# Kernel optimization log

Hardware: AMD Instinct MI355X
Metric: run time of the kernel (lower is better)

## Reference

```python
import jax, jax.numpy as jnp
import numpy as np

CUTOFF = 5.0
NUM_RADIAL = 6
HIDDEN = 128
N_NODES = 100000
N_EDGES = 800000
MAX_Z = 95
P = 6  # envelope_exponent(5) + 1, per PyG Envelope


def _envelope(x):
    # PyG DimeNet Envelope: (1/x + a*x^(p-1) + b*x^p + c*x^(p+1)) * (x < 1)
    a = -(P + 1) * (P + 2) / 2.0   # -28
    b = P * (P + 2)                # 48
    c = -P * (P + 1) / 2.0         # -21
    xp0 = x ** (P - 1)
    xp1 = xp0 * x
    xp2 = xp1 * x
    return (1.0 / x + a * xp0 + b * xp1 + c * xp2) * (x < 1.0)


def setup_inputs():
    key = jax.random.key(0)
    ks = jax.random.split(key, 8)
    z = jax.random.randint(ks[0], (N_NODES,), 0, MAX_Z, dtype=jnp.int32)
    pos = jax.random.normal(ks[1], (N_NODES, 3), dtype=jnp.float32)
    ei = jax.random.randint(ks[2], (2, N_EDGES), 0, N_NODES, dtype=jnp.int32)
    i, j = ei[0], ei[1]
    j = jnp.where(j == i, (j + 1) % N_NODES, j)  # radius_graph emits no self-loops (avoids d=0)
    edge_index = jnp.stack([i, j])
    # BesselBasisLayer learnable frequencies: pi * n
    freq = np.pi * jnp.arange(1, NUM_RADIAL + 1, dtype=jnp.float32)
    s3 = float(np.sqrt(3.0))
    emb_table = jax.random.uniform(ks[3], (MAX_Z, HIDDEN), jnp.float32, -s3, s3)
    W_rbf = jax.random.normal(ks[4], (NUM_RADIAL, HIDDEN), jnp.float32) * (1.0 / np.sqrt(NUM_RADIAL))
    b_rbf = jnp.zeros((HIDDEN,), jnp.float32)
    W_lin = jax.random.normal(ks[5], (3 * HIDDEN, HIDDEN), jnp.float32) * (1.0 / np.sqrt(3 * HIDDEN))
    b_lin = jnp.zeros((HIDDEN,), jnp.float32)
    return {"z": z, "pos": pos, "edge_index": edge_index, "freq": freq,
            "emb_table": emb_table, "W_rbf": W_rbf, "b_rbf": b_rbf,
            "W_lin": W_lin, "b_lin": b_lin}


def reference(z, pos, edge_index, freq, emb_table, W_rbf, b_rbf, W_lin, b_lin):
    n = z.shape[0]
    i, j = edge_index[0], edge_index[1]
    # per-edge distance  [E]
    d = jnp.sqrt(jnp.sum((pos[i] - pos[j]) ** 2, axis=-1))
    # Bessel RBF  [E, num_radial]
    x = d[:, None] / CUTOFF
    rbf = _envelope(x) * jnp.sin(freq * x)
    # DimeNet EmbeddingBlock (act = SiLU/swish)
    h_rbf = jax.nn.silu(rbf @ W_rbf + b_rbf)            # [E, H]
    xz = emb_table[z]                                    # [N, H]
    e_emb = jax.nn.silu(
        jnp.concatenate([xz[i], xz[j], h_rbf], axis=-1) @ W_lin + b_lin
    )                                                    # [E, H]
    # scatter_mean over target node j -> [N, H]
    sums = jax.ops.segment_sum(e_emb, j, num_segments=n)
    cnt = jax.ops.segment_sum(jnp.ones_like(d), j, num_segments=n)
    v_emb = sums / jnp.maximum(cnt, 1.0)[:, None]
    return v_emb  # pool=None -> node-level embeddings
```

## Files before the change

### kernel.cpp

```cpp
#include <hip/hip_runtime.h>
#include <hip/hip_bf16.h>
#include <math.h>

#define HID 128
#define NRAD 6
#define TABN 4096
#define CUTOFF_INV 0.2f
#define MZ 95
#define MZP (MZ + 1)
#define SENTI (MZ << 13)
#define PAD 32
#define OVF_CAP 65536
#define FTR 8
#define LOG2E 1.4426950408889634f
#define LN2   0.6931471805599453f

typedef unsigned int uint32;
typedef __attribute__((ext_vector_type(2))) float f2;

__global__ void zpack_k(const float* __restrict__ pos, const int* __restrict__ z,
                        float4* __restrict__ pos4, int* __restrict__ cnt,
                        int* __restrict__ ovfcnt, int N) {
    int n = blockIdx.x * 256 + threadIdx.x;
    if (blockIdx.x == 0 && threadIdx.x == 0) *ovfcnt = 0;
    if (n < N) {
        float4 p;
        p.x = pos[3 * n];
        p.y = pos[3 * n + 1];
        p.z = pos[3 * n + 2];
        p.w = __int_as_float(z[n]);
        pos4[n] = p;
        cnt[n]  = 0;
    }
}

__global__ void build1(const float* __restrict__ emb, const float* __restrict__ W_lin,
                       const float* __restrict__ freq, const float* __restrict__ W_rbf,
                       const float* __restrict__ b_rbf, const float* __restrict__ b_lin,
                       const int* __restrict__ ei, const float4* __restrict__ pos4,
                       __hip_bfloat16* __restrict__ Tb, float* __restrict__ ftab,
                       int* __restrict__ cnt, int* __restrict__ payload,
                       int* __restrict__ ovfcnt, int2* __restrict__ ovfbuf,
                       int MAXZ, int E) {
    __shared__ float sh[FTR * HID];
    int h   = threadIdx.x;
    int bid = blockIdx.x;
    int nT  = 2 * (MAXZ + 1);
    int nF  = (TABN + FTR) / FTR;
    if (bid < nT) {
        int zz = bid >> 1, s = bid & 1;
        if (zz == MAXZ) {
            Tb[(size_t)(s * (MAXZ + 1) + zz) * HID + h] = __float2bfloat16(-86.5f);
            return;
        }
        sh[h] = emb[zz * HID + h];
        __syncthreads();
        const float* W = W_lin + (size_t)s * HID * HID;
        float acc = (s == 0) ? b_lin[h] : 0.f;
#pragma unroll 8
        for (int k = 0; k < HID; ++k) acc = fmaf(sh[k], W[k * HID + h], acc);
        Tb[(size_t)(s * (MAXZ + 1) + zz) * HID + h] = __float2bfloat16(acc * LOG2E);
    } else if (bid < nT + nF) {
        int t0 = (bid - nT) * FTR;
        for (int r = 0; r < FTR; ++r) {
            int t = t0 + r;
            float rbf[NRAD];
            if (t == 0) {
#pragma unroll
                for (int k = 0; k < NRAD; ++k) rbf[k] = freq[k];
            } else if (t >= TABN) {
#pragma unroll
                for (int k = 0; k < NRAD; ++k) rbf[k] = 0.f;
            } else {
                float x  = (float)t / (float)TABN;
                float x2 = x * x, x5 = x2 * x2 * x;
                float env = 1.f / x + x5 * (-28.f + x * (48.f + x * (-21.f)));
#pragma unroll
                for (int k = 0; k < NRAD; ++k) rbf[k] = env * sinf(freq[k] * x);
            }
            float pre = b_rbf[h];
#pragma unroll
            for (int k = 0; k < NRAD; ++k) pre = fmaf(rbf[k], W_rbf[k * HID + h], pre);
            sh[r * HID + h] = pre / (1.f + __expf(-pre));
        }
        __syncthreads();
        const float* W3 = W_lin + (size_t)2 * HID * HID;
        float acc[FTR];
#pragma unroll
        for (int r = 0; r < FTR; ++r) acc[r] = 0.f;
#pragma unroll 4
        for (int k = 0; k < HID; ++k) {
            float w = W3[k * HID + h];
#pragma unroll
            for (int r = 0; r < FTR; ++r) acc[r] = fmaf(sh[r * HID + k], w, acc[r]);
        }
        for (int r = 0; r < FTR; ++r) {
            int t = t0 + r;
            if (t <= TABN) ftab[(size_t)t * HID + h] = acc[r] * LOG2E;
        }
    } else {
        int t  = (bid - nT - nF) * HID + h;
        int Eh = (E + 1) >> 1;
        if (t < Eh) {
            int  e1   = t + Eh;
            bool has1 = e1 < E;
            int i0 = ei[t],  j0 = ei[E + t];
            int i1 = has1 ? ei[e1] : i0, j1 = has1 ? ei[E + e1] : j0;
            float4 a0 = pos4[i0], b0 = pos4[j0];
            float4 a1 = pos4[i1], b1 = pos4[j1];

            float dx0 = a0.x - b0.x, dy0 = a0.y - b0.y, dz0 = a0.z - b0.z;
            float d0  = sqrtf(dx0 * dx0 + dy0 * dy0 + dz0 * dz0);
            float u0  = fminf(d0 * CUTOFF_INV, 1.0f) * (float)TABN;
            int   ti0 = (int)(u0 + 0.5f);
            if (ti0 > TABN) ti0 = TABN;
            int pl0 = ti0 | (__float_as_int(a0.w) << 13);
            int r0  = atomicAdd(&cnt[j0], 1);
            if (r0 < PAD) payload[(size_t)j0 * PAD + r0] = pl0;
            else { int o = atomicAdd(ovfcnt, 1); if (o < OVF_CAP) ovfbuf[o] = make_int2(j0, pl0); }

            if (has1) {
                float dx1 = a1.x - b1.x, dy1 = a1.y - b1.y, dz1 = a1.z - b1.z;
                float d1  = sqrtf(dx1 * dx1 + dy1 * dy1 + dz1 * dz1);
                float u1  = fminf(d1 * CUTOFF_INV, 1.0f) * (float)TABN;
                int   ti1 = (int)(u1 + 0.5f);
                if (ti1 > TABN) ti1 = TABN;
                int pl1 = ti1 | (__float_as_int(a1.w) << 13);
                int r1  = atomicAdd(&cnt[j1], 1);
                if (r1 < PAD) payload[(size_t)j1 * PAD + r1] = pl1;
                else { int o = atomicAdd(ovfcnt, 1); if (o < OVF_CAP) ovfbuf[o] = make_int2(j1, pl1); }
            }
        }
    }
}

__device__ __forceinline__ float exp2neg(float x) {
    float r; asm("v_exp_f32 %0, -%1" : "=v"(r) : "v"(x)); return r;
}

#define RL(pv_, idx_) __builtin_amdgcn_readlane((pv_), (idx_))

#define FLOAD(pl_) (*(const f2*)((const char*)ftab + (uint32)((((pl_) & 0x1FFF) << 9) + fbyte)))

#define TLA(pl_) sT[((((pl_) >> 13) & 0x7F) << 6) + lane]

#define COMPUTE(f_, ua_) do {                                                  \
    f2 A_, P_, E_, R_;                                                         \
    A_.x = __uint_as_float((ua_) << 16);                                       \
    A_.y = __uint_as_float((ua_) & 0xFFFF0000u);                               \
    P_ = (A_ + Bv) + f_;                                  \
    E_.x = exp2neg(P_.x);  E_.y = exp2neg(P_.y);                               \
    E_ = E_ + onev;                                              \
    R_.x = __builtin_amdgcn_rcpf(E_.x);                                        \
    R_.y = __builtin_amdgcn_rcpf(E_.y);                                        \
    acc = __builtin_elementwise_fma(P_, R_, acc);            \
} while (0)

__launch_bounds__(1024)
__global__ void gather_k(const int* __restrict__ cnt, const int* __restrict__ payload,
                         const uint32* __restrict__ Tb32, const float* __restrict__ ftab,
                         const int* __restrict__ z,
                         const int* __restrict__ ovfcnt, const int2* __restrict__ ovfbuf,
                         float* __restrict__ out, int N) {
    __shared__ uint32 sT[MZP * (HID / 2)];
    int tid = threadIdx.x;
    for (int k = tid; k < MZP * (HID / 2); k += 1024) sT[k] = Tb32[k];
    __syncthreads();

    const uint32* T2g = Tb32 + MZP * (HID / 2);
    int lane = tid & 63;
    int l32  = lane & 31;
    int wv   = __builtin_amdgcn_readfirstlane(tid >> 6);
    uint32 fbyte = (uint32)lane << 3;
    f2 onev; onev.x = 1.f; onev.y = 1.f;
    int nov  = __builtin_amdgcn_readfirstlane(*ovfcnt);
    if (nov > OVF_CAP) nov = OVF_CAP;
    int nW = gridDim.x << 4;

    int n = (blockIdx.x << 4) + wv;
    int degC = 0, plvC = SENTI; uint32 ubC = 0;
    if (n < N) {
        degC = __builtin_amdgcn_readfirstlane(cnt[n]);
        plvC = payload[(size_t)n * PAD + l32];
        int zn = __builtin_amdgcn_readfirstlane(z[n]);
        ubC  = T2g[(zn << 6) + lane];
    }

    while (n < N) {
        int n2 = n + nW;
        int degN = 0, plvN = SENTI; uint32 ubN = 0;
        if (n2 < N) {
            degN = __builtin_amdgcn_readfirstlane(cnt[n2]);
            plvN = payload[(size_t)n2 * PAD + l32];
            int zn2 = __builtin_amdgcn_readfirstlane(z[n2]);
            ubN  = T2g[(zn2 << 6) + lane];
        }

        int deg = degC;
        int cb  = deg < PAD ? deg : PAD;
        int plv = (l32 < cb) ? plvC : SENTI;
        f2 Bv;
        Bv.x = __uint_as_float(ubC << 16);
        Bv.y = __uint_as_float(ubC & 0xFFFF0000u);

        f2 acc; acc.x = 0.f; acc.y = 0.f;
        if (cb > 0) {
            int pl0 = RL(plv, 0), pl1 = RL(plv, 1), pl2 = RL(plv, 2);
            f2 g0 = FLOAD(pl0), g1 = FLOAD(pl1), g2 = FLOAD(pl2);
            uint32 ua0 = TLA(pl0);
            uint32 ua1 = TLA(pl1);
#pragma unroll 4
            for (int k = 0; k < cb; ++k) {
                int pl3 = RL(plv, k + 3);
                f2 g3 = FLOAD(pl3);
                uint32 ua2 = TLA(pl2);
                COMPUTE(g0, ua0);
                g0 = g1; g1 = g2; g2 = g3;
                ua0 = ua1; ua1 = ua2;
                pl2 = pl3;
            }
        }
        if (deg > PAD && nov > 0) {
            for (int o = 0; o < nov; ++o) {
                int2 v = ovfbuf[o];
                int jn = __builtin_amdgcn_readfirstlane(v.x);
                if (jn == n) {
                    int pl = __builtin_amdgcn_readfirstlane(v.y);
                    f2 f_ = FLOAD(pl);
                    uint32 ua_ = TLA(pl);
                    COMPUTE(f_, ua_);
                }
            }
        }
        float s = (deg > 0) ? LN2 / (float)deg : 0.0f;
        f2 o2; o2.x = acc.x * s; o2.y = acc.y * s;
        *(f2*)(out + (size_t)n * HID + (lane << 1)) = o2;
        n = n2; degC = degN; plvC = plvN; ubC = ubN;
    }
}

extern "C" void kernel_launch(void* const* d_in, const int* in_sizes, int n_in,
                              void* d_out, int out_size, void* d_ws, size_t ws_size,
                              hipStream_t stream) {
    const int*   z     = (const int*)d_in[0];
    const float* pos   = (const float*)d_in[1];
    const int*   ei    = (const int*)d_in[2];
    const float* freq  = (const float*)d_in[3];
    const float* emb   = (const float*)d_in[4];
    const float* W_rbf = (const float*)d_in[5];
    const float* b_rbf = (const float*)d_in[6];
    const float* W_lin = (const float*)d_in[7];
    const float* b_lin = (const float*)d_in[8];

    int N    = in_sizes[0];
    int E    = in_sizes[2] / 2;
    int MAXZ = in_sizes[4] / HID;
    float* out = (float*)d_out;

    int N_pad = ((N + 1024) / 1024) * 1024;

    char* ws = (char*)d_ws;
    size_t off = 0;
    auto alloc = [&](size_t bytes) { char* p = ws + off; off = (off + bytes + 255) & ~(size_t)255; return p; };
    int*   cnt     = (int*)alloc((size_t)N_pad * 4);
    int*   ovfcnt  = (int*)alloc(256);
    __hip_bfloat16* Tb = (__hip_bfloat16*)alloc((size_t)2 * (MAXZ + 1) * HID * 2);
    float* ftab    = (float*)alloc((size_t)(TABN + 1) * HID * 4);
    int*   payload = (int*)alloc((size_t)N_pad * PAD * 4);
    int2*  ovfbuf  = (int2*)alloc((size_t)OVF_CAP * 8);
    float4* pos4   = (float4*)alloc((size_t)N_pad * 16);

    zpack_k<<<(N + 255) / 256, 256, 0, stream>>>(pos, z, pos4, cnt, ovfcnt, N);

    int Eh = (E + 1) / 2;
    int nBuild = 2 * (MAXZ + 1) + (TABN + FTR) / FTR + (Eh + HID - 1) / HID;
    build1<<<nBuild, HID, 0, stream>>>(emb, W_lin, freq, W_rbf, b_rbf, b_lin,
                                       ei, pos4, Tb, ftab, cnt, payload,
                                       ovfcnt, ovfbuf, MAXZ, E);
    gather_k<<<512, 1024, 0, stream>>>(cnt, payload, (const uint32*)Tb, ftab, z,
                                       ovfcnt, ovfbuf, out, N);
}
```

Baseline: 180.3 us.

## Pack atom type into count word and deepen gather prefetch pipeline

The node's atom type is stored in the top byte of the per-node counter, so the gather kernel no longer makes a separate dependent load of z per node. The gather loop now prefetches two nodes ahead: counts and payload two iterations out, and the bias row plus first ftab row one iteration out. This is meant to hide global-load latency at node boundaries. It adds register pressure and relies on degrees staying below 2^24.

After: 175.4 us (median of 2 runs). 1.03x faster.

```diff
diff --git a/kernel.cpp b/kernel.cpp
--- a/kernel.cpp
+++ b/kernel.cpp
@@ -24,13 +24,14 @@
     int n = blockIdx.x * 256 + threadIdx.x;
     if (blockIdx.x == 0 && threadIdx.x == 0) *ovfcnt = 0;
     if (n < N) {
+        int zn = z[n];
         float4 p;
         p.x = pos[3 * n];
         p.y = pos[3 * n + 1];
         p.z = pos[3 * n + 2];
-        p.w = __int_as_float(z[n]);
+        p.w = __int_as_float(zn);
         pos4[n] = p;
-        cnt[n]  = 0;
+        cnt[n]  = zn << 24;
     }
 }
 
@@ -115,7 +116,7 @@
             int   ti0 = (int)(u0 + 0.5f);
             if (ti0 > TABN) ti0 = TABN;
             int pl0 = ti0 | (__float_as_int(a0.w) << 13);
-            int r0  = atomicAdd(&cnt[j0], 1);
+            int r0  = atomicAdd(&cnt[j0], 1) & 0xFFFFFF;
             if (r0 < PAD) payload[(size_t)j0 * PAD + r0] = pl0;
             else { int o = atomicAdd(ovfcnt, 1); if (o < OVF_CAP) ovfbuf[o] = make_int2(j0, pl0); }
 
@@ -126,7 +127,7 @@
                 int   ti1 = (int)(u1 + 0.5f);
                 if (ti1 > TABN) ti1 = TABN;
                 int pl1 = ti1 | (__float_as_int(a1.w) << 13);
-                int r1  = atomicAdd(&cnt[j1], 1);
+                int r1  = atomicAdd(&cnt[j1], 1) & 0xFFFFFF;
                 if (r1 < PAD) payload[(size_t)j1 * PAD + r1] = pl1;
                 else { int o = atomicAdd(ovfcnt, 1); if (o < OVF_CAP) ovfbuf[o] = make_int2(j1, pl1); }
             }
@@ -159,7 +160,6 @@
 __launch_bounds__(1024)
 __global__ void gather_k(const int* __restrict__ cnt, const int* __restrict__ payload,
                          const uint32* __restrict__ Tb32, const float* __restrict__ ftab,
-                         const int* __restrict__ z,
                          const int* __restrict__ ovfcnt, const int2* __restrict__ ovfbuf,
                          float* __restrict__ out, int N) {
     __shared__ uint32 sT[MZP * (HID / 2)];
@@ -177,50 +177,64 @@
     if (nov > OVF_CAP) nov = OVF_CAP;
     int nW = gridDim.x << 4;
 
-    int n = (blockIdx.x << 4) + wv;
-    int degC = 0, plvC = SENTI; uint32 ubC = 0;
+    int n  = (blockIdx.x << 4) + wv;
+    int n1 = n + nW;
+
+    int cv0 = 0, plv0 = SENTI; uint32 ub0 = 0;
     if (n < N) {
-        degC = __builtin_amdgcn_readfirstlane(cnt[n]);
-        plvC = payload[(size_t)n * PAD + l32];
-        int zn = __builtin_amdgcn_readfirstlane(z[n]);
-        ubC  = T2g[(zn << 6) + lane];
+        cv0  = __builtin_amdgcn_readfirstlane(cnt[n]);
+        plv0 = payload[(size_t)n * PAD + l32];
+    }
+    int deg0 = cv0 & 0xFFFFFF;
+    int zn0  = ((uint32)cv0) >> 24;
+    int cb0  = deg0 < PAD ? deg0 : PAD;
+    plv0 = (l32 < cb0) ? plv0 : SENTI;
+    if (n < N) ub0 = T2g[(zn0 << 6) + lane];
+    f2 g00 = FLOAD(RL(plv0, 0));
+
+    int cv1 = 0, plv1 = SENTI;
+    if (n1 < N) {
+        cv1  = __builtin_amdgcn_readfirstlane(cnt[n1]);
+        plv1 = payload[(size_t)n1 * PAD + l32];
     }
 
     while (n < N) {
-        int n2 = n + nW;
-        int degN = 0, plvN = SENTI; uint32 ubN = 0;
+        int n2 = n1 + nW;
+        int cv2 = 0, plv2 = SENTI;
         if (n2 < N) {
-            degN = __builtin_amdgcn_readfirstlane(cnt[n2]);
-            plvN = payload[(size_t)n2 * PAD + l32];
-            int zn2 = __builtin_amdgcn_readfirstlane(z[n2]);
-            ubN  = T2g[(zn2 << 6) + lane];
-        }
-
-        int deg = degC;
-        int cb  = deg < PAD ? deg : PAD;
-        int plv = (l32 < cb) ? plvC : SENTI;
+            cv2  = __builtin_amdgcn_readfirstlane(cnt[n2]);
+            plv2 = payload[(size_t)n2 * PAD + l32];
+        }
+        int deg1 = cv1 & 0xFFFFFF;
+        int zn1  = ((uint32)cv1) >> 24;
+        int cb1  = deg1 < PAD ? deg1 : PAD;
+        plv1 = (l32 < cb1) ? plv1 : SENTI;
+        uint32 ub1 = 0;
+        if (n1 < N) ub1 = T2g[(zn1 << 6) + lane];
+        f2 g01 = FLOAD(RL(plv1, 0));
+
         f2 Bv;
-        Bv.x = __uint_as_float(ubC << 16);
-        Bv.y = __uint_as_float(ubC & 0xFFFF0000u);
-
+        Bv.x = __uint_as_float(ub0 << 16);
+        Bv.y = __uint_as_float(ub0 & 0xFFFF0000u);
         f2 acc; acc.x = 0.f; acc.y = 0.f;
-        if (cb > 0) {
-            int pl0 = RL(plv, 0), pl1 = RL(plv, 1), pl2 = RL(plv, 2);
-            f2 g0 = FLOAD(pl0), g1 = FLOAD(pl1), g2 = FLOAD(pl2);
-            uint32 ua0 = TLA(pl0);
-            uint32 ua1 = TLA(pl1);
+        if (cb0 > 0) {
+            f2 g0 = g00;
+            int pl1e = RL(plv0, 1), pl2e = RL(plv0, 2);
+            f2 g1 = FLOAD(pl1e), g2 = FLOAD(pl2e);
+            uint32 ua0 = TLA(RL(plv0, 0));
+            uint32 ua1 = TLA(pl1e);
 #pragma unroll 4
-            for (int k = 0; k < cb; ++k) {
-                int pl3 = RL(plv, k + 3);
+            for (int k = 0; k < cb0; ++k) {
+                int pl3 = RL(plv0, k + 3);
                 f2 g3 = FLOAD(pl3);
-                uint32 ua2 = TLA(pl2);
+                uint32 ua2 = TLA(pl2e);
                 COMPUTE(g0, ua0);
                 g0 = g1; g1 = g2; g2 = g3;
                 ua0 = ua1; ua1 = ua2;
-                pl2 = pl3;
-            }
-        }
-        if (deg > PAD && nov > 0) {
+                pl2e = pl3;
+            }
+        }
+        if (deg0 > PAD && nov > 0) {
             for (int o = 0; o < nov; ++o) {
                 int2 v = ovfbuf[o];
                 int jn = __builtin_amdgcn_readfirstlane(v.x);
@@ -232,10 +246,13 @@
                 }
             }
         }
-        float s = (deg > 0) ? LN2 / (float)deg : 0.0f;
+        float s = (deg0 > 0) ? LN2 / (float)deg0 : 0.0f;
         f2 o2; o2.x = acc.x * s; o2.y = acc.y * s;
         *(f2*)(out + (size_t)n * HID + (lane << 1)) = o2;
-        n = n2; degC = degN; plvC = plvN; ubC = ubN;
+
+        n = n1; n1 = n2;
+        deg0 = deg1; cb0 = cb1; plv0 = plv1; ub0 = ub1; g00 = g01;
+        cv1 = cv2; plv1 = plv2;
     }
 }
 
@@ -277,6 +294,6 @@
     build1<<<nBuild, HID, 0, stream>>>(emb, W_lin, freq, W_rbf, b_rbf, b_lin,
                                        ei, pos4, Tb, ftab, cnt, payload,
                                        ovfcnt, ovfbuf, MAXZ, E);
-    gather_k<<<512, 1024, 0, stream>>>(cnt, payload, (const uint32*)Tb, ftab, z,
+    gather_k<<<512, 1024, 0, stream>>>(cnt, payload, (const uint32*)Tb, ftab,
                                        ovfcnt, ovfbuf, out, N);
 }
```

## Process two nodes per wave in gather, pack z into count, four edges per build thread

Applied to the files above, without the earlier changes.

The gather kernel now interleaves two destination nodes per wavefront, with deeper software prefetch of counts and payloads two iterations ahead, so the exp/rcp chains of the two nodes can overlap memory latency. The atomic-counter word now carries the node's atomic number in its top byte, which removes the separate z load in gather. The edge build phase handles four edges per thread and issues all atomics before the payload stores. Costs are higher register pressure (launch bounds set to 8 waves), load imbalance when the two nodes have different degrees, and a degree field that is now limited to 24 bits.

Result: slower. 185.2 us (+2.7%).

```diff
diff --git a/kernel.cpp b/kernel.cpp
--- a/kernel.cpp
+++ b/kernel.cpp
@@ -24,14 +24,24 @@
     int n = blockIdx.x * 256 + threadIdx.x;
     if (blockIdx.x == 0 && threadIdx.x == 0) *ovfcnt = 0;
     if (n < N) {
+        int zn = z[n];
         float4 p;
         p.x = pos[3 * n];
         p.y = pos[3 * n + 1];
         p.z = pos[3 * n + 2];
-        p.w = __int_as_float(z[n]);
+        p.w = __int_as_float(zn);
         pos4[n] = p;
-        cnt[n]  = 0;
+        cnt[n]  = zn << 24;
     }
+}
+
+__device__ __forceinline__ int mk_pl(float4 a, float4 b) {
+    float dx = a.x - b.x, dy = a.y - b.y, dz = a.z - b.z;
+    float d  = sqrtf(dx * dx + dy * dy + dz * dz);
+    float u  = fminf(d * CUTOFF_INV, 1.0f) * (float)TABN;
+    int   ti = (int)(u + 0.5f);
+    if (ti > TABN) ti = TABN;
+    return ti | (__float_as_int(a.w) << 13);
 }
 
 __global__ void build1(const float* __restrict__ emb, const float* __restrict__ W_lin,
@@ -100,36 +110,38 @@
         }
     } else {
         int t  = (bid - nT - nF) * HID + h;
-        int Eh = (E + 1) >> 1;
-        if (t < Eh) {
-            int  e1   = t + Eh;
-            bool has1 = e1 < E;
+        int Eq = (E + 3) >> 2;
+        if (t < Eq) {
+            int e1 = t + Eq, e2 = t + 2 * Eq, e3 = t + 3 * Eq;
+            bool h1 = e1 < E, h2 = e2 < E, h3 = e3 < E;
             int i0 = ei[t],  j0 = ei[E + t];
-            int i1 = has1 ? ei[e1] : i0, j1 = has1 ? ei[E + e1] : j0;
+            int i1 = h1 ? ei[e1] : i0, j1 = h1 ? ei[E + e1] : j0;
+            int i2 = h2 ? ei[e2] : i0, j2 = h2 ? ei[E + e2] : j0;
+            int i3 = h3 ? ei[e3] : i0, j3 = h3 ? ei[E + e3] : j0;
             float4 a0 = pos4[i0], b0 = pos4[j0];
             float4 a1 = pos4[i1], b1 = pos4[j1];
-
-            float dx0 = a0.x - b0.x, dy0 = a0.y - b0.y, dz0 = a0.z - b0.z;
-            float d0  = sqrtf(dx0 * dx0 + dy0 * dy0 + dz0 * dz0);
-            float u0  = fminf(d0 * CUTOFF_INV, 1.0f) * (float)TABN;
-            int   ti0 = (int)(u0 + 0.5f);
-            if (ti0 > TABN) ti0 = TABN;
-            int pl0 = ti0 | (__float_as_int(a0.w) << 13);
-            int r0  = atomicAdd(&cnt[j0], 1);
+            float4 a2 = pos4[i2], b2 = pos4[j2];
+            float4 a3 = pos4[i3], b3 = pos4[j3];
+            int pl0 = mk_pl(a0, b0), pl1 = mk_pl(a1, b1);
+            int pl2 = mk_pl(a2, b2), pl3 = mk_pl(a3, b3);
+            int r0 =      atomicAdd(&cnt[j0], 1) & 0xFFFFFF;
+            int r1 = h1 ? atomicAdd(&cnt[j1], 1) & 0xFFFFFF : 0;
+            int r2 = h2 ? atomicAdd(&cnt[j2], 1) & 0xFFFFFF : 0;
+            int r3 = h3 ? atomicAdd(&cnt[j3], 1) & 0xFFFFFF : 0;
             if (r0 < PAD) payload[(size_t)j0 * PAD + r0] = pl0;
             else { int o = atomicAdd(ovfcnt, 1); if (o < OVF_CAP) ovfbuf[o] = make_int2(j0, pl0); }
-
-            if (has1) {
-                float dx1 = a1.x - b1.x, dy1 = a1.y - b1.y, dz1 = a1.z - b1.z;
-                float d1  = sqrtf(dx1 * dx1 + dy1 * dy1 + dz1 * dz1);
-                float u1  = fminf(d1 * CUTOFF_INV, 1.0f) * (float)TABN;
-                int   ti1 = (int)(u1 + 0.5f);
-                if (ti1 > TABN) ti1 = TABN;
-                int pl1 = ti1 | (__float_as_int(a1.w) << 13);
-                int r1  = atomicAdd(&cnt[j1], 1);
+            if (h1) {
                 if (r1 < PAD) payload[(size_t)j1 * PAD + r1] = pl1;
                 else { int o = atomicAdd(ovfcnt, 1); if (o < OVF_CAP) ovfbuf[o] = make_int2(j1, pl1); }
             }
+            if (h2) {
+                if (r2 < PAD) payload[(size_t)j2 * PAD + r2] = pl2;
+                else { int o = atomicAdd(ovfcnt, 1); if (o < OVF_CAP) ovfbuf[o] = make_int2(j2, pl2); }
+            }
+            if (h3) {
+                if (r3 < PAD) payload[(size_t)j3 * PAD + r3] = pl3;
+                else { int o = atomicAdd(ovfcnt, 1); if (o < OVF_CAP) ovfbuf[o] = make_int2(j3, pl3); }
+            }
         }
     }
 }
@@ -144,22 +156,21 @@
 
 #define TLA(pl_) sT[((((pl_) >> 13) & 0x7F) << 6) + lane]
 
-#define COMPUTE(f_, ua_) do {                                                  \
+#define COMPUTE(f_, ua_, Bv_, acc_) do {                                       \
     f2 A_, P_, E_, R_;                                                         \
     A_.x = __uint_as_float((ua_) << 16);                                       \
     A_.y = __uint_as_float((ua_) & 0xFFFF0000u);                               \
-    P_ = (A_ + Bv) + f_;                                  \
+    P_ = (A_ + Bv_) + f_;                                 \
     E_.x = exp2neg(P_.x);  E_.y = exp2neg(P_.y);                               \
     E_ = E_ + onev;                                              \
     R_.x = __builtin_amdgcn_rcpf(E_.x);                                        \
     R_.y = __builtin_amdgcn_rcpf(E_.y);                                        \
-    acc = __builtin_elementwise_fma(P_, R_, acc);            \
+    acc_ = __builtin_elementwise_fma(P_, R_, acc_);          \
 } while (0)
 
-__launch_bounds__(1024)
+__launch_bounds__(1024, 8)
 __global__ void gather_k(const int* __restrict__ cnt, const int* __restrict__ payload,
                          const uint32* __restrict__ Tb32, const float* __restrict__ ftab,
-                         const int* __restrict__ z,
                          const int* __restrict__ ovfcnt, const int2* __restrict__ ovfbuf,
                          float* __restrict__ out, int N) {
     __shared__ uint32 sT[MZP * (HID / 2)];
@@ -175,67 +186,100 @@
     f2 onev; onev.x = 1.f; onev.y = 1.f;
     int nov  = __builtin_amdgcn_readfirstlane(*ovfcnt);
     if (nov > OVF_CAP) nov = OVF_CAP;
-    int nW = gridDim.x << 4;
-
-    int n = (blockIdx.x << 4) + wv;
-    int degC = 0, plvC = SENTI; uint32 ubC = 0;
-    if (n < N) {
-        degC = __builtin_amdgcn_readfirstlane(cnt[n]);
-        plvC = payload[(size_t)n * PAD + l32];
-        int zn = __builtin_amdgcn_readfirstlane(z[n]);
-        ubC  = T2g[(zn << 6) + lane];
-    }
-
-    while (n < N) {
-        int n2 = n + nW;
-        int degN = 0, plvN = SENTI; uint32 ubN = 0;
-        if (n2 < N) {
-            degN = __builtin_amdgcn_readfirstlane(cnt[n2]);
-            plvN = payload[(size_t)n2 * PAD + l32];
-            int zn2 = __builtin_amdgcn_readfirstlane(z[n2]);
-            ubN  = T2g[(zn2 << 6) + lane];
-        }
-
-        int deg = degC;
-        int cb  = deg < PAD ? deg : PAD;
-        int plv = (l32 < cb) ? plvC : SENTI;
-        f2 Bv;
-        Bv.x = __uint_as_float(ubC << 16);
-        Bv.y = __uint_as_float(ubC & 0xFFFF0000u);
-
-        f2 acc; acc.x = 0.f; acc.y = 0.f;
-        if (cb > 0) {
-            int pl0 = RL(plv, 0), pl1 = RL(plv, 1), pl2 = RL(plv, 2);
-            f2 g0 = FLOAD(pl0), g1 = FLOAD(pl1), g2 = FLOAD(pl2);
-            uint32 ua0 = TLA(pl0);
-            uint32 ua1 = TLA(pl1);
-#pragma unroll 4
-            for (int k = 0; k < cb; ++k) {
-                int pl3 = RL(plv, k + 3);
-                f2 g3 = FLOAD(pl3);
-                uint32 ua2 = TLA(pl2);
-                COMPUTE(g0, ua0);
-                g0 = g1; g1 = g2; g2 = g3;
-                ua0 = ua1; ua1 = ua2;
-                pl2 = pl3;
-            }
-        }
-        if (deg > PAD && nov > 0) {
+    int nW  = gridDim.x << 4;
+    int nW2 = nW << 1;
+
+    int nA = (blockIdx.x << 4) + wv;
+    int nB = nA + nW;
+
+    int cvA = 0, cvB = 0, plvA = SENTI, plvB = SENTI;
+    if (nA < N) { cvA = __builtin_amdgcn_readfirstlane(cnt[nA]); plvA = payload[(size_t)nA * PAD + l32]; }
+    if (nB < N) { cvB = __builtin_amdgcn_readfirstlane(cnt[nB]); plvB = payload[(size_t)nB * PAD + l32]; }
+    int degA = cvA & 0xFFFFFF, degB = cvB & 0xFFFFFF;
+    int cbA = degA < PAD ? degA : PAD, cbB = degB < PAD ? degB : PAD;
+    plvA = (l32 < cbA) ? plvA : SENTI;
+    plvB = (l32 < cbB) ? plvB : SENTI;
+    uint32 ubA = 0, ubB = 0;
+    if (nA < N) ubA = T2g[((((uint32)cvA) >> 24) << 6) + lane];
+    if (nB < N) ubB = T2g[((((uint32)cvB) >> 24) << 6) + lane];
+    f2 gA00 = FLOAD(RL(plvA, 0));
+    f2 gB00 = FLOAD(RL(plvB, 0));
+
+    int nA1 = nA + nW2, nB1 = nB + nW2;
+    int cvA1 = 0, cvB1 = 0, plvA1 = SENTI, plvB1 = SENTI;
+    if (nA1 < N) { cvA1 = __builtin_amdgcn_readfirstlane(cnt[nA1]); plvA1 = payload[(size_t)nA1 * PAD + l32]; }
+    if (nB1 < N) { cvB1 = __builtin_amdgcn_readfirstlane(cnt[nB1]); plvB1 = payload[(size_t)nB1 * PAD + l32]; }
+
+    while (nA < N) {
+        int nA2 = nA1 + nW2, nB2 = nB1 + nW2;
+        int cvA2 = 0, cvB2 = 0, plvA2 = SENTI, plvB2 = SENTI;
+        if (nA2 < N) { cvA2 = __builtin_amdgcn_readfirstlane(cnt[nA2]); plvA2 = payload[(size_t)nA2 * PAD + l32]; }
+        if (nB2 < N) { cvB2 = __builtin_amdgcn_readfirstlane(cnt[nB2]); plvB2 = payload[(size_t)nB2 * PAD + l32]; }
+        int degA1 = cvA1 & 0xFFFFFF, degB1 = cvB1 & 0xFFFFFF;
+        int cbA1 = degA1 < PAD ? degA1 : PAD, cbB1 = degB1 < PAD ? degB1 : PAD;
+        plvA1 = (l32 < cbA1) ? plvA1 : SENTI;
+        plvB1 = (l32 < cbB1) ? plvB1 : SENTI;
+        uint32 ubA1 = 0, ubB1 = 0;
+        if (nA1 < N) ubA1 = T2g[((((uint32)cvA1) >> 24) << 6) + lane];
+        if (nB1 < N) ubB1 = T2g[((((uint32)cvB1) >> 24) << 6) + lane];
+        f2 gA01 = FLOAD(RL(plvA1, 0));
+        f2 gB01 = FLOAD(RL(plvB1, 0));
+
+        f2 BvA, BvB;
+        BvA.x = __uint_as_float(ubA << 16); BvA.y = __uint_as_float(ubA & 0xFFFF0000u);
+        BvB.x = __uint_as_float(ubB << 16); BvB.y = __uint_as_float(ubB & 0xFFFF0000u);
+        f2 accA; accA.x = 0.f; accA.y = 0.f;
+        f2 accB; accB.x = 0.f; accB.y = 0.f;
+        int cbm = cbA > cbB ? cbA : cbB;
+        if (cbm > 0) {
+            int plA1e = RL(plvA, 1), plB1e = RL(plvB, 1);
+            int plA2e = RL(plvA, 2), plB2e = RL(plvB, 2);
+            f2 gA0 = gA00, gB0 = gB00;
+            f2 gA1 = FLOAD(plA1e), gB1 = FLOAD(plB1e);
+            f2 gA2 = FLOAD(plA2e), gB2 = FLOAD(plB2e);
+            uint32 uaA0 = TLA(RL(plvA, 0)), uaB0 = TLA(RL(plvB, 0));
+            uint32 uaA1 = TLA(plA1e),       uaB1 = TLA(plB1e);
+#pragma unroll 2
+            for (int k = 0; k < cbm; ++k) {
+                int plA3 = RL(plvA, k + 3), plB3 = RL(plvB, k + 3);
+                f2 gA3 = FLOAD(plA3), gB3 = FLOAD(plB3);
+                uint32 uaA2 = TLA(plA2e), uaB2 = TLA(plB2e);
+                COMPUTE(gA0, uaA0, BvA, accA);
+                COMPUTE(gB0, uaB0, BvB, accB);
+                gA0 = gA1; gA1 = gA2; gA2 = gA3;
+                gB0 = gB1; gB1 = gB2; gB2 = gB3;
+                uaA0 = uaA1; uaA1 = uaA2;
+                uaB0 = uaB1; uaB1 = uaB2;
+                plA2e = plA3; plB2e = plB3;
+            }
+        }
+        if ((degA > PAD || degB > PAD) && nov > 0) {
             for (int o = 0; o < nov; ++o) {
                 int2 v = ovfbuf[o];
                 int jn = __builtin_amdgcn_readfirstlane(v.x);
-                if (jn == n) {
+                if (jn == nA || jn == nB) {
                     int pl = __builtin_amdgcn_readfirstlane(v.y);
                     f2 f_ = FLOAD(pl);
                     uint32 ua_ = TLA(pl);
-                    COMPUTE(f_, ua_);
+                    if (jn == nA) COMPUTE(f_, ua_, BvA, accA);
+                    else          COMPUTE(f_, ua_, BvB, accB);
                 }
             }
         }
-        float s = (deg > 0) ? LN2 / (float)deg : 0.0f;
-        f2 o2; o2.x = acc.x * s; o2.y = acc.y * s;
-        *(f2*)(out + (size_t)n * HID + (lane << 1)) = o2;
-        n = n2; degC = degN; plvC = plvN; ubC = ubN;
+        float sA = (degA > 0) ? LN2 / (float)degA : 0.0f;
+        f2 oA; oA.x = accA.x * sA; oA.y = accA.y * sA;
+        *(f2*)(out + (size_t)nA * HID + (lane << 1)) = oA;
+        if (nB < N) {
+            float sB = (degB > 0) ? LN2 / (float)degB : 0.0f;
+            f2 oB; oB.x = accB.x * sB; oB.y = accB.y * sB;
+            *(f2*)(out + (size_t)nB * HID + (lane << 1)) = oB;
+        }
+
+        nA = nA1; nB = nB1; nA1 = nA2; nB1 = nB2;
+        degA = degA1; degB = degB1; cbA = cbA1; cbB = cbB1;
+        plvA = plvA1; plvB = plvB1; ubA = ubA1; ubB = ubB1;
+        gA00 = gA01; gB00 = gB01;
+        cvA1 = cvA2; cvB1 = cvB2; plvA1 = plvA2; plvB1 = plvB2;
     }
 }
 
@@ -272,11 +316,11 @@
 
     zpack_k<<<(N + 255) / 256, 256, 0, stream>>>(pos, z, pos4, cnt, ovfcnt, N);
 
-    int Eh = (E + 1) / 2;
-    int nBuild = 2 * (MAXZ + 1) + (TABN + FTR) / FTR + (Eh + HID - 1) / HID;
+    int Eq = (E + 3) / 4;
+    int nBuild = 2 * (MAXZ + 1) + (TABN + FTR) / FTR + (Eq + HID - 1) / HID;
     build1<<<nBuild, HID, 0, stream>>>(emb, W_lin, freq, W_rbf, b_rbf, b_lin,
                                        ei, pos4, Tb, ftab, cnt, payload,
                                        ovfcnt, ovfbuf, MAXZ, E);
-    gather_k<<<512, 1024, 0, stream>>>(cnt, payload, (const uint32*)Tb, ftab, z,
+    gather_k<<<512, 1024, 0, stream>>>(cnt, payload, (const uint32*)Tb, ftab,
                                        ovfcnt, ovfbuf, out, N);
 }
```
